# Performance work log

Measured on AMD Instinct MI355X. Metric: run time of the kernel, lower is better.

The kernel has to match this reference:

```python
import jax, jax.numpy as jnp
import numpy as np

B, H, W = 4, 256, 256
DIM, DIM_OUT, NUM_HEADS = 96, 192, 3
WS = 8            # window_size
QS = 2            # q_stride (2,2)
HIDDEN = int(DIM_OUT * 4.0)
EPS = 1e-6


def layernorm(x, g, b):
    m = jnp.mean(x, axis=-1, keepdims=True)
    v = jnp.mean(jnp.square(x - m), axis=-1, keepdims=True)
    return (x - m) * jax.lax.rsqrt(v + EPS) * g + b


def maxpool2x2(x):
    # x: [..., h, w, c] -> [..., h//2, w//2, c]
    s = x.shape
    x = x.reshape(s[:-3] + (s[-3] // QS, QS, s[-2] // QS, QS, s[-1]))
    return x.max(axis=(-4, -2))


def setup_inputs() -> dict:
    key = jax.random.key(0)
    ks = jax.random.split(key, 16)
    std = 0.02
    return {
        "x": jax.random.normal(ks[0], (B, H, W, DIM), dtype=jnp.float32),
        "norm1_g": jnp.ones((DIM,), jnp.float32),
        "norm1_b": jnp.zeros((DIM,), jnp.float32),
        "proj_w": jax.random.normal(ks[1], (DIM, DIM_OUT), jnp.float32) * std,
        "proj_b": jnp.zeros((DIM_OUT,), jnp.float32),
        "qkv_w": jax.random.normal(ks[2], (DIM, 3 * DIM_OUT), jnp.float32) * std,
        "qkv_b": jnp.zeros((3 * DIM_OUT,), jnp.float32),
        "attn_proj_w": jax.random.normal(ks[3], (DIM_OUT, DIM_OUT), jnp.float32) * std,
        "attn_proj_b": jnp.zeros((DIM_OUT,), jnp.float32),
        "norm2_g": jnp.ones((DIM_OUT,), jnp.float32),
        "norm2_b": jnp.zeros((DIM_OUT,), jnp.float32),
        "mlp_w1": jax.random.normal(ks[4], (DIM_OUT, HIDDEN), jnp.float32) * std,
        "mlp_b1": jnp.zeros((HIDDEN,), jnp.float32),
        "mlp_w2": jax.random.normal(ks[5], (HIDDEN, DIM_OUT), jnp.float32) * std,
        "mlp_b2": jnpp_zeros if False else jnp.zeros((DIM_OUT,), jnp.float32),
    }


def reference(x, norm1_g, norm1_b, proj_w, proj_b, qkv_w, qkv_b,
              attn_proj_w, attn_proj_b, norm2_g, norm2_b,
              mlp_w1, mlp_b1, mlp_w2, mlp_b2):
    b, h, w, _ = x.shape
    xn = layernorm(x, norm1_g, norm1_b)

    # dim != dim_out: shortcut = proj(norm(x)), then pooled by q_stride
    shortcut = xn @ proj_w + proj_b                       # [B,H,W,Do]
    shortcut = maxpool2x2(shortcut)                       # [B,H/2,W/2,Do]

    # window partition (H,W divisible by WS -> no padding)
    nh, nw = h // WS, w // WS
    xw = xn.reshape(b, nh, WS, nw, WS, DIM).transpose(0, 1, 3, 2, 4, 5)
    xw = xw.reshape(b * nh * nw, WS, WS, DIM)             # [Bw,WS,WS,C]
    Bw = xw.shape[0]

    # MultiScaleAttention with q pooling
    hd = DIM_OUT // NUM_HEADS
    qkv = (xw @ qkv_w + qkv_b).reshape(Bw, WS * WS, 3, NUM_HEADS, hd)
    q, k, v = qkv[:, :, 0], qkv[:, :, 1], qkv[:, :, 2]    # [Bw,N,h,d]
    q = maxpool2x2(q.reshape(Bw, WS, WS, DIM_OUT))        # [Bw,WS/2,WS/2,Do]
    wq = WS // QS
    q = q.reshape(Bw, wq * wq, NUM_HEADS, hd)

    scale = 1.0 / jnp.sqrt(jnp.asarray(hd, x.dtype))
    scores = jnp.einsum('bqhd,bkhd->bhqk', q, k) * scale
    probs = jax.nn.softmax(scores, axis=-1)
    out = jnp.einsum('bhqk,bkhd->bqhd', probs, v).reshape(Bw, wq, wq, DIM_OUT)
    out = out @ attn_proj_w + attn_proj_b                 # [Bw,wq,wq,Do]

    # window unpartition at pooled resolution
    hp, wp = h // QS, w // QS
    out = out.reshape(b, nh, nw, wq, wq, DIM_OUT).transpose(0, 1, 3, 2, 4, 5)
    out = out.reshape(b, hp, wp, DIM_OUT)

    y = shortcut + out
    yn = layernorm(y, norm2_g, norm2_b)
    mlp = jax.nn.gelu(yn @ mlp_w1 + mlp_b1, approximate=False) @ mlp_w2 + mlp_b2
    return y + mlp
```

## Files before the change

kernel.cpp:

```cpp
#include <hip/hip_runtime.h>
#include <hip/hip_bf16.h>
#include <math.h>

#define EPSV 1e-6f

typedef __attribute__((ext_vector_type(8))) short bf16x8;
typedef __attribute__((ext_vector_type(4))) float f32x4;
typedef __attribute__((ext_vector_type(4))) unsigned short u16x4;

__device__ inline float bf2f(unsigned short u) {
  union { unsigned int i; float f; } v;
  v.i = ((unsigned int)u) << 16;
  return v.f;
}
__device__ inline unsigned short f2bf(float f) {
  unsigned int u = __builtin_bit_cast(unsigned int, f);
  u += 0x7FFFu + ((u >> 16) & 1u);
  return (unsigned short)(u >> 16);
}
__device__ inline float fast_gelu(float v) {
  float u = 1.5957691216057308f * (v + 0.044715f * v * v * v);
  float t = __expf(-u);
  return v * __builtin_amdgcn_rcpf(1.f + t);
}

__global__ __launch_bounds__(256) void k0_pack(
    const float* __restrict__ qw, const float* __restrict__ aw,
    const float* __restrict__ w1, const float* __restrict__ w2,
    const float* __restrict__ pw, unsigned short* __restrict__ qwp,
    unsigned short* __restrict__ awp, unsigned short* __restrict__ w1p,
    unsigned short* __restrict__ w2p, unsigned short* __restrict__ pwp) {
  int idx = blockIdx.x * 256 + threadIdx.x;
  int lane = idx & 63;
  int l15 = lane & 15, quad = lane >> 4;
  if (idx < 6912) {
    int fi = idx >> 6;
    int ntile = fi / 3, kstep = fi - ntile * 3;
    int n = ntile * 16 + l15, k0 = kstep * 32 + quad * 8;
#pragma unroll
    for (int j = 0; j < 8; ++j)
      qwp[(size_t)idx * 8 + j] = f2bf(qw[(size_t)(k0 + j) * 576 + n]);
  } else if (idx < 11520) {
    int i2 = idx - 6912;
    int fi = i2 >> 6;
    int ntile = fi / 6, kstep = fi - ntile * 6;
    int n = ntile * 16 + l15, k0 = kstep * 32 + quad * 8;
#pragma unroll
    for (int j = 0; j < 8; ++j)
      awp[(size_t)i2 * 8 + j] = f2bf(aw[(size_t)(k0 + j) * 192 + n]);
  } else if (idx < 29952) {
    int i3 = idx - 11520;
    int fi = i3 >> 6;
    int ntile = fi / 6, kstep = fi - ntile * 6;
    int n = ntile * 16 + l15, k0 = kstep * 32 + quad * 8;
#pragma unroll
    for (int j = 0; j < 8; ++j)
      w1p[(size_t)i3 * 8 + j] = f2bf(w1[(size_t)(k0 + j) * 768 + n]);
  } else if (idx < 48384) {
    int i4 = idx - 29952;
    int fi = i4 >> 6;
    int ntile = fi / 24, kstep = fi - ntile * 24;
    int n = ntile * 16 + l15, k0 = kstep * 32 + quad * 8;
#pragma unroll
    for (int j = 0; j < 8; ++j)
      w2p[(size_t)i4 * 8 + j] = f2bf(w2[(size_t)(k0 + j) * 192 + n]);
  } else if (idx < 50688) {
    int i5 = idx - 48384;
    int fi = i5 >> 6;
    int ntile = fi / 3, kstep = fi - ntile * 3;
    int n = ntile * 16 + l15, k0 = kstep * 32 + quad * 8;
#pragma unroll
    for (int j = 0; j < 8; ++j)
      pwp[(size_t)i5 * 8 + j] = f2bf(pw[(size_t)(k0 + j) * 192 + n]);
  }
}

__global__ __launch_bounds__(256) void k1234_fused(
    const float* __restrict__ x, const float* __restrict__ n1g,
    const float* __restrict__ n1b, const unsigned short* __restrict__ pwp,
    const float* __restrict__ pb, const unsigned short* __restrict__ qwp,
    const float* __restrict__ qb, const unsigned short* __restrict__ awp,
    const float* __restrict__ ab, const float* __restrict__ n2g,
    const float* __restrict__ n2b, const unsigned short* __restrict__ w1p,
    const float* __restrict__ b1, const unsigned short* __restrict__ w2p,
    const float* __restrict__ b2, float* __restrict__ out) {
  __shared__ __align__(16) unsigned char smem[46848];
  unsigned short (*kk)[200] = (unsigned short (*)[200])smem;
  unsigned short (*vT)[72] = (unsigned short (*)[72])smem;
  unsigned short (*wbuf)[16][72] =
      (unsigned short (*)[16][72])(smem + 27648);
  float (*sc)[192] = (float (*)[192])(smem + 34560);
  unsigned short (*yn)[200] = (unsigned short (*)[200])(smem + 6400);
  unsigned short (*hls)[200] = (unsigned short (*)[200])(smem + 12800);

  int tid = threadIdx.x, wave = tid >> 6, lane = tid & 63;
  int wi = blockIdx.x;
  int b = wi >> 10, nh = (wi >> 5) & 31, nw = wi & 31;
  int grow0 = nh * 8, gcol0 = nw * 8;
  int l15 = lane & 15, quad = lane >> 4;

  {
    int tt = tid >> 2, sub = tid & 3;
    int rr = tt >> 3, cc = tt & 7;
    size_t tok = (size_t)((b * 256 + grow0 + rr) * 256 + gcol0 + cc);
    const f32x4* xr4 = (const f32x4*)(x + tok * 96 + sub * 24);
    f32x4 v[6];
#pragma unroll
    for (int i = 0; i < 6; ++i) v[i] = xr4[i];
    float s = 0.f;
#pragma unroll
    for (int i = 0; i < 6; ++i)
#pragma unroll
      for (int j = 0; j < 4; ++j) s += v[i][j];
    s += __shfl_xor(s, 1);
    s += __shfl_xor(s, 2);
    float mean = s * (1.f / 96.f);
    float q = 0.f;
#pragma unroll
    for (int i = 0; i < 6; ++i)
#pragma unroll
      for (int j = 0; j < 4; ++j) {
        float d = v[i][j] - mean;
        q += d * d;
      }
    q += __shfl_xor(q, 1);
    q += __shfl_xor(q, 2);
    float rstd = rsqrtf(q * (1.f / 96.f) + EPSV);
    const f32x4* g4 = (const f32x4*)(n1g + sub * 24);
    const f32x4* b4 = (const f32x4*)(n1b + sub * 24);
#pragma unroll
    for (int i = 0; i < 6; ++i) {
      f32x4 gg = g4[i], bb = b4[i];
      u16x4 o;
#pragma unroll
      for (int j = 0; j < 4; ++j)
        o[j] = f2bf((v[i][j] - mean) * rstd * gg[j] + bb[j]);
      *(u16x4*)(&kk[tt][sub * 24 + i * 4]) = o;
    }
  }
  __syncthreads();

  bf16x8 areg[4][3];
#pragma unroll
  for (int mt = 0; mt < 4; ++mt)
#pragma unroll
    for (int ks = 0; ks < 3; ++ks)
      areg[mt][ks] = *(const bf16x8*)(&kk[mt * 16 + l15][ks * 32 + quad * 8]);
  __syncthreads();

#pragma unroll
  for (int nl = 0; nl < 3; ++nl) {
    int nt = wave * 3 + nl;
    const unsigned short* bp = pwp + ((size_t)(nt * 3) * 64 + lane) * 8;
    bf16x8 b0 = *(const bf16x8*)(bp);
    bf16x8 b1v = *(const bf16x8*)(bp + 512);
    bf16x8 b2v = *(const bf16x8*)(bp + 1024);
    int c = nt * 16 + l15;
    float bias = pb[c];
#pragma unroll
    for (int mt = 0; mt < 4; ++mt) {
      f32x4 acc = {0.f, 0.f, 0.f, 0.f};
      acc = __builtin_amdgcn_mfma_f32_16x16x32_bf16(areg[mt][0], b0, acc, 0, 0, 0);
      acc = __builtin_amdgcn_mfma_f32_16x16x32_bf16(areg[mt][1], b1v, acc, 0, 0, 0);
      acc = __builtin_amdgcn_mfma_f32_16x16x32_bf16(areg[mt][2], b2v, acc, 0, 0, 0);
      float p0 = fmaxf(acc[0], acc[1]);
      float p1 = fmaxf(acc[2], acc[3]);
      float q0 = fmaxf(p0, __shfl_xor(p0, 32));
      float q1 = fmaxf(p1, __shfl_xor(p1, 32));
      if (quad < 2) {
        int p = mt * 4 + quad * 2;
        sc[p][c] = q0 + bias;
        sc[p + 1][c] = q1 + bias;
      }
    }
  }

#pragma unroll
  for (int aj = 0; aj < 6; ++aj) {
    int type, hh, nt;
    if (wave < 3) {
      if (aj < 4) { type = 0; hh = wave; nt = aj; }
      else { int kidx = wave * 2 + (aj - 4); type = 1; hh = kidx >> 2; nt = kidx & 3; }
    } else {
      int kidx = 6 + aj; type = 1; hh = kidx >> 2; nt = kidx & 3;
    }
    int gnt = type * 12 + hh * 4 + nt;
    const unsigned short* bp = qwp + (size_t)gnt * 1536 + lane * 8;
    bf16x8 b0 = *(const bf16x8*)(bp);
    bf16x8 b1v = *(const bf16x8*)(bp + 512);
    bf16x8 b2v = *(const bf16x8*)(bp + 1024);
    int dloc = nt * 16 + l15;
    int dglob = hh * 64 + dloc;
    float bias = qb[type * 192 + dglob];
#pragma unroll
    for (int mt = 0; mt < 4; ++mt) {
      f32x4 acc = {0.f, 0.f, 0.f, 0.f};
      acc = __builtin_amdgcn_mfma_f32_16x16x32_bf16(areg[mt][0], b0, acc, 0, 0, 0);
      acc = __builtin_amdgcn_mfma_f32_16x16x32_bf16(areg[mt][1], b1v, acc, 0, 0, 0);
      acc = __builtin_amdgcn_mfma_f32_16x16x32_bf16(areg[mt][2], b2v, acc, 0, 0, 0);
      if (type == 0) {
        float p0 = fmaxf(acc[0], acc[1]);
        float p1 = fmaxf(acc[2], acc[3]);
        float q0 = fmaxf(p0, __shfl_xor(p0, 32));
        float q1 = fmaxf(p1, __shfl_xor(p1, 32));
        if (quad < 2) {
          int p = mt * 4 + quad * 2;
          wbuf[wave][p][dloc] = f2bf(q0 + bias);
          wbuf[wave][p + 1][dloc] = f2bf(q1 + bias);
        }
      } else {
        int t0 = mt * 16 + quad * 4;
#pragma unroll
        for (int r = 0; r < 4; ++r) kk[t0 + r][dglob] = f2bf(acc[r] + bias);
      }
    }
  }
  __syncthreads();

  f32x4 s4[4];
  if (wave < 3) {
    int h = wave;
    bf16x8 aq0 = *(const bf16x8*)(&wbuf[wave][l15][quad * 8]);
    bf16x8 aq1 = *(const bf16x8*)(&wbuf[wave][l15][32 + quad * 8]);
#pragma unroll
    for (int kt = 0; kt < 4; ++kt) {
      bf16x8 bk0 = *(const bf16x8*)(&kk[kt * 16 + l15][h * 64 + quad * 8]);
      bf16x8 bk1 = *(const bf16x8*)(&kk[kt * 16 + l15][h * 64 + 32 + quad * 8]);
      f32x4 s = {0.f, 0.f, 0.f, 0.f};
      s = __builtin_amdgcn_mfma_f32_16x16x32_bf16(aq0, bk0, s, 0, 0, 0);
      s = __builtin_amdgcn_mfma_f32_16x16x32_bf16(aq1, bk1, s, 0, 0, 0);
      s4[kt] = s;
    }
  }
  __syncthreads();

#pragma unroll
  for (int vj = 0; vj < 3; ++vj) {
    int vidx = wave * 3 + vj;
    int hh = vidx >> 2, nt = vidx & 3;
    const unsigned short* bp =
        qwp + (size_t)(24 + hh * 4 + nt) * 1536 + lane * 8;
    bf16x8 b0 = *(const bf16x8*)(bp);
    bf16x8 b1v = *(const bf16x8*)(bp + 512);
    bf16x8 b2v = *(const bf16x8*)(bp + 1024);
    int dglob = hh * 64 + nt * 16 + l15;
    float bias = qb[384 + dglob];
#pragma unroll
    for (int mt = 0; mt < 4; ++mt) {
      f32x4 acc = {0.f, 0.f, 0.f, 0.f};
      acc = __builtin_amdgcn_mfma_f32_16x16x32_bf16(areg[mt][0], b0, acc, 0, 0, 0);
      acc = __builtin_amdgcn_mfma_f32_16x16x32_bf16(areg[mt][1], b1v, acc, 0, 0, 0);
      acc = __builtin_amdgcn_mfma_f32_16x16x32_bf16(areg[mt][2], b2v, acc, 0, 0, 0);
      int t0 = mt * 16 + quad * 4;
      u16x4 pk;
#pragma unroll
      for (int r = 0; r < 4; ++r) pk[r] = f2bf(acc[r] + bias);
      *(u16x4*)(&vT[dglob][t0]) = pk;
    }
  }

  if (wave < 3) {
    float ps[4][4];
#pragma unroll
    for (int r = 0; r < 4; ++r) {
      float m = fmaxf(fmaxf(s4[0][r], s4[1][r]), fmaxf(s4[2][r], s4[3][r]));
#pragma unroll
      for (int o = 8; o; o >>= 1) m = fmaxf(m, __shfl_xor(m, o));
      float sm = 0.f;
#pragma unroll
      for (int kt = 0; kt < 4; ++kt) {
        float e = __expf((s4[kt][r] - m) * 0.125f);
        ps[kt][r] = e;
        sm += e;
      }
#pragma unroll
      for (int o = 8; o; o >>= 1) sm += __shfl_xor(sm, o);
      float inv = __builtin_amdgcn_rcpf(sm);
#pragma unroll
      for (int kt = 0; kt < 4; ++kt) ps[kt][r] *= inv;
    }
#pragma unroll
    for (int kt = 0; kt < 4; ++kt)
#pragma unroll
      for (int r = 0; r < 4; ++r)
        wbuf[wave][quad * 4 + r][kt * 16 + l15] = f2bf(ps[kt][r]);
  }
  __syncthreads();

  f32x4 o4[4];
  if (wave < 3) {
    int h = wave;
    bf16x8 ap0 = *(const bf16x8*)(&wbuf[wave][l15][quad * 8]);
    bf16x8 ap1 = *(const bf16x8*)(&wbuf[wave][l15][32 + quad * 8]);
#pragma unroll
    for (int dt = 0; dt < 4; ++dt) {
      bf16x8 bv0 = *(const bf16x8*)(&vT[h * 64 + dt * 16 + l15][quad * 8]);
      bf16x8 bv1 = *(const bf16x8*)(&vT[h * 64 + dt * 16 + l15][32 + quad * 8]);
      f32x4 o = {0.f, 0.f, 0.f, 0.f};
      o = __builtin_amdgcn_mfma_f32_16x16x32_bf16(ap0, bv0, o, 0, 0, 0);
      o = __builtin_amdgcn_mfma_f32_16x16x32_bf16(ap1, bv1, o, 0, 0, 0);
      o4[dt] = o;
    }
  }
  __syncthreads();

  if (wave < 3) {
    int h = wave;
#pragma unroll
    for (int dt = 0; dt < 4; ++dt)
#pragma unroll
      for (int r = 0; r < 4; ++r)
        kk[quad * 4 + r][h * 64 + dt * 16 + l15] = f2bf(o4[dt][r]);
  }
  __syncthreads();

  bf16x8 ao[6];
#pragma unroll
  for (int ks = 0; ks < 6; ++ks)
    ao[ks] = *(const bf16x8*)(&kk[l15][ks * 32 + quad * 8]);
#pragma unroll
  for (int nl = 0; nl < 3; ++nl) {
    int ntl = wave * 3 + nl;
    const unsigned short* bp = awp + (size_t)ntl * 3072 + lane * 8;
    f32x4 acc = {0.f, 0.f, 0.f, 0.f};
#pragma unroll
    for (int ks = 0; ks < 6; ++ks) {
      bf16x8 bw = *(const bf16x8*)(bp + ks * 512);
      acc = __builtin_amdgcn_mfma_f32_16x16x32_bf16(ao[ks], bw, acc, 0, 0, 0);
    }
    int cc = ntl * 16 + l15;
    float bias = ab[cc];
#pragma unroll
    for (int r = 0; r < 4; ++r) {
      int p = quad * 4 + r;
      sc[p][cc] += acc[r] + bias;
    }
  }
  __syncthreads();

  {
    int tt = wave * 4 + quad;
    const f32x4* y4 = (const f32x4*)(&sc[tt][l15 * 12]);
    f32x4 vv[3];
    vv[0] = y4[0]; vv[1] = y4[1]; vv[2] = y4[2];
    float s = 0.f;
#pragma unroll
    for (int i = 0; i < 3; ++i)
#pragma unroll
      for (int j = 0; j < 4; ++j) s += vv[i][j];
    s += __shfl_xor(s, 1);
    s += __shfl_xor(s, 2);
    s += __shfl_xor(s, 4);
    s += __shfl_xor(s, 8);
    float mean = s * (1.f / 192.f);
    float q = 0.f;
#pragma unroll
    for (int i = 0; i < 3; ++i)
#pragma unroll
      for (int j = 0; j < 4; ++j) {
        float d = vv[i][j] - mean;
        q += d * d;
      }
    q += __shfl_xor(q, 1);
    q += __shfl_xor(q, 2);
    q += __shfl_xor(q, 4);
    q += __shfl_xor(q, 8);
    float rstd = rsqrtf(q * (1.f / 192.f) + EPSV);
    const f32x4* g4 = (const f32x4*)(n2g + l15 * 12);
    const f32x4* b4 = (const f32x4*)(n2b + l15 * 12);
#pragma unroll
    for (int i = 0; i < 3; ++i) {
      f32x4 gg = g4[i], bb = b4[i];
      u16x4 o;
#pragma unroll
      for (int j = 0; j < 4; ++j)
        o[j] = f2bf((vv[i][j] - mean) * rstd * gg[j] + bb[j]);
      *(u16x4*)(&yn[tt][l15 * 12 + i * 4]) = o;
    }
  }
  __syncthreads();

  bf16x8 ar[6];
#pragma unroll
  for (int ks = 0; ks < 6; ++ks)
    ar[ks] = *(const bf16x8*)(&yn[l15][ks * 32 + quad * 8]);

  f32x4 acc2[3];
#pragma unroll
  for (int nl = 0; nl < 3; ++nl) acc2[nl] = (f32x4){0.f, 0.f, 0.f, 0.f};

  for (int c = 0; c < 4; ++c) {
#pragma unroll
    for (int nl = 0; nl < 3; ++nl) {
      int gnt = c * 12 + wave * 3 + nl;
      const unsigned short* bp = w1p + ((size_t)(gnt * 6) * 64 + lane) * 8;
      f32x4 t0 = {0.f, 0.f, 0.f, 0.f};
#pragma unroll
      for (int ks = 0; ks < 6; ++ks) {
        bf16x8 bw = *(const bf16x8*)(bp + ks * 512);
        t0 = __builtin_amdgcn_mfma_f32_16x16x32_bf16(ar[ks], bw, t0, 0, 0, 0);
      }
      int lcol = wave * 48 + nl * 16 + l15;
      float bias = b1[c * 192 + lcol];
#pragma unroll
      for (int r = 0; r < 4; ++r)
        hls[quad * 4 + r][lcol] = f2bf(fast_gelu(t0[r] + bias));
    }
    __syncthreads();
    bf16x8 hr[6];
#pragma unroll
    for (int ks = 0; ks < 6; ++ks)
      hr[ks] = *(const bf16x8*)(&hls[l15][ks * 32 + quad * 8]);
#pragma unroll
    for (int nl = 0; nl < 3; ++nl) {
      int nt2 = wave * 3 + nl;
      const unsigned short* bp =
          w2p + ((size_t)(nt2 * 24 + c * 6) * 64 + lane) * 8;
#pragma unroll
      for (int ks = 0; ks < 6; ++ks) {
        bf16x8 bw = *(const bf16x8*)(bp + ks * 512);
        acc2[nl] =
            __builtin_amdgcn_mfma_f32_16x16x32_bf16(hr[ks], bw, acc2[nl], 0, 0, 0);
      }
    }
    __syncthreads();
  }

#pragma unroll
  for (int nl = 0; nl < 3; ++nl) {
    int col = (wave * 3 + nl) * 16 + l15;
    float bias = b2[col];
#pragma unroll
    for (int r = 0; r < 4; ++r) {
      int p = quad * 4 + r;
      int hp = nh * 4 + (p >> 2), wp2 = nw * 4 + (p & 3);
      size_t oi = ((size_t)((b * 128 + hp) * 128 + wp2)) * 192 + col;
      out[oi] = sc[p][col] + acc2[nl][r] + bias;
    }
  }
}

extern "C" void kernel_launch(void* const* d_in, const int* in_sizes, int n_in,
                              void* d_out, int out_size, void* d_ws,
                              size_t ws_size, hipStream_t stream) {
  const float* x = (const float*)d_in[0];
  const float* n1g = (const float*)d_in[1];
  const float* n1b = (const float*)d_in[2];
  const float* pw = (const float*)d_in[3];
  const float* pb = (const float*)d_in[4];
  const float* qw = (const float*)d_in[5];
  const float* qb = (const float*)d_in[6];
  const float* aw = (const float*)d_in[7];
  const float* ab = (const float*)d_in[8];
  const float* n2g = (const float*)d_in[9];
  const float* n2b = (const float*)d_in[10];
  const float* w1 = (const float*)d_in[11];
  const float* b1 = (const float*)d_in[12];
  const float* w2 = (const float*)d_in[13];
  const float* b2 = (const float*)d_in[14];
  float* out = (float*)d_out;

  char* wsb = (char*)d_ws;
  unsigned short* qwp = (unsigned short*)wsb;
  unsigned short* awp = (unsigned short*)(wsb + 110592);
  unsigned short* w1p = (unsigned short*)(wsb + 184320);
  unsigned short* w2p = (unsigned short*)(wsb + 479232);
  unsigned short* pwp = (unsigned short*)(wsb + 774144);

  hipLaunchKernelGGL(k0_pack, dim3(198), dim3(256), 0, stream, qw, aw, w1, w2,
                     pw, qwp, awp, w1p, w2p, pwp);
  hipLaunchKernelGGL(k1234_fused, dim3(4096), dim3(256), 0, stream, x, n1g,
                     n1b, pwp, pb, qwp, qb, awp, ab, n2g, n2b, w1p, b1, w2p,
                     b2, out);
}
```

Before: 317.8 us.

## Use hardware packed bf16 conversion and shrink LDS to fit more blocks

Replaces the software round-to-nearest f32-to-bf16 conversion with the v_cvt_pk_bf16_f32 instruction, which converts two values at once, at every staging point. The shortcut projection results are held in registers and written to LDS later, so the score buffer can alias the wbuf region and the shared allocation drops from 46848 to 39936 bytes. Launch bounds now request 4 blocks per CU to raise occupancy. The cost is extra live registers for the held shortcut values, under a tighter register budget that could cause spills.

```diff
diff --git a/kernel.cpp b/kernel.cpp
--- a/kernel.cpp
+++ b/kernel.cpp
@@ -7,6 +7,7 @@
 typedef __attribute__((ext_vector_type(8))) short bf16x8;
 typedef __attribute__((ext_vector_type(4))) float f32x4;
 typedef __attribute__((ext_vector_type(4))) unsigned short u16x4;
+typedef __attribute__((ext_vector_type(2))) unsigned int u32x2;
 
 __device__ inline float bf2f(unsigned short u) {
   union { unsigned int i; float f; } v;
@@ -17,6 +18,11 @@
   unsigned int u = __builtin_bit_cast(unsigned int, f);
   u += 0x7FFFu + ((u >> 16) & 1u);
   return (unsigned short)(u >> 16);
+}
+__device__ inline unsigned int pk2(float lo, float hi) {
+  unsigned int r;
+  asm("v_cvt_pk_bf16_f32 %0, %1, %2" : "=v"(r) : "v"(lo), "v"(hi));
+  return r;
 }
 __device__ inline float fast_gelu(float v) {
   float u = 1.5957691216057308f * (v + 0.044715f * v * v * v);
@@ -75,7 +81,7 @@
   }
 }
 
-__global__ __launch_bounds__(256) void k1234_fused(
+__global__ __launch_bounds__(256, 4) void k1234_fused(
     const float* __restrict__ x, const float* __restrict__ n1g,
     const float* __restrict__ n1b, const unsigned short* __restrict__ pwp,
     const float* __restrict__ pb, const unsigned short* __restrict__ qwp,
@@ -84,14 +90,14 @@
     const float* __restrict__ n2b, const unsigned short* __restrict__ w1p,
     const float* __restrict__ b1, const unsigned short* __restrict__ w2p,
     const float* __restrict__ b2, float* __restrict__ out) {
-  __shared__ __align__(16) unsigned char smem[46848];
+  __shared__ __align__(16) unsigned char smem[39936];
   unsigned short (*kk)[200] = (unsigned short (*)[200])smem;
   unsigned short (*vT)[72] = (unsigned short (*)[72])smem;
+  unsigned short (*yn)[200] = (unsigned short (*)[200])(smem + 6400);
+  unsigned short (*hls)[200] = (unsigned short (*)[200])(smem + 12800);
   unsigned short (*wbuf)[16][72] =
       (unsigned short (*)[16][72])(smem + 27648);
-  float (*sc)[192] = (float (*)[192])(smem + 34560);
-  unsigned short (*yn)[200] = (unsigned short (*)[200])(smem + 6400);
-  unsigned short (*hls)[200] = (unsigned short (*)[200])(smem + 12800);
+  float (*sc)[192] = (float (*)[192])(smem + 27648);
 
   int tid = threadIdx.x, wave = tid >> 6, lane = tid & 63;
   int wi = blockIdx.x;
@@ -131,11 +137,12 @@
 #pragma unroll
     for (int i = 0; i < 6; ++i) {
       f32x4 gg = g4[i], bb = b4[i];
-      u16x4 o;
-#pragma unroll
-      for (int j = 0; j < 4; ++j)
-        o[j] = f2bf((v[i][j] - mean) * rstd * gg[j] + bb[j]);
-      *(u16x4*)(&kk[tt][sub * 24 + i * 4]) = o;
+      u32x2 w;
+      w[0] = pk2((v[i][0] - mean) * rstd * gg[0] + bb[0],
+                 (v[i][1] - mean) * rstd * gg[1] + bb[1]);
+      w[1] = pk2((v[i][2] - mean) * rstd * gg[2] + bb[2],
+                 (v[i][3] - mean) * rstd * gg[3] + bb[3]);
+      *(u32x2*)(&kk[tt][sub * 24 + i * 4]) = w;
     }
   }
   __syncthreads();
@@ -148,6 +155,7 @@
       areg[mt][ks] = *(const bf16x8*)(&kk[mt * 16 + l15][ks * 32 + quad * 8]);
   __syncthreads();
 
+  float scr[3][4][2];
 #pragma unroll
   for (int nl = 0; nl < 3; ++nl) {
     int nt = wave * 3 + nl;
@@ -155,8 +163,7 @@
     bf16x8 b0 = *(const bf16x8*)(bp);
     bf16x8 b1v = *(const bf16x8*)(bp + 512);
     bf16x8 b2v = *(const bf16x8*)(bp + 1024);
-    int c = nt * 16 + l15;
-    float bias = pb[c];
+    float bias = pb[nt * 16 + l15];
 #pragma unroll
     for (int mt = 0; mt < 4; ++mt) {
       f32x4 acc = {0.f, 0.f, 0.f, 0.f};
@@ -165,13 +172,8 @@
       acc = __builtin_amdgcn_mfma_f32_16x16x32_bf16(areg[mt][2], b2v, acc, 0, 0, 0);
       float p0 = fmaxf(acc[0], acc[1]);
       float p1 = fmaxf(acc[2], acc[3]);
-      float q0 = fmaxf(p0, __shfl_xor(p0, 32));
-      float q1 = fmaxf(p1, __shfl_xor(p1, 32));
-      if (quad < 2) {
-        int p = mt * 4 + quad * 2;
-        sc[p][c] = q0 + bias;
-        sc[p + 1][c] = q1 + bias;
-      }
+      scr[nl][mt][0] = fmaxf(p0, __shfl_xor(p0, 32)) + bias;
+      scr[nl][mt][1] = fmaxf(p1, __shfl_xor(p1, 32)) + bias;
     }
   }
 
@@ -203,15 +205,20 @@
         float p1 = fmaxf(acc[2], acc[3]);
         float q0 = fmaxf(p0, __shfl_xor(p0, 32));
         float q1 = fmaxf(p1, __shfl_xor(p1, 32));
+        unsigned int uq = pk2(q0 + bias, q1 + bias);
         if (quad < 2) {
           int p = mt * 4 + quad * 2;
-          wbuf[wave][p][dloc] = f2bf(q0 + bias);
-          wbuf[wave][p + 1][dloc] = f2bf(q1 + bias);
+          wbuf[wave][p][dloc] = (unsigned short)uq;
+          wbuf[wave][p + 1][dloc] = (unsigned short)(uq >> 16);
         }
       } else {
         int t0 = mt * 16 + quad * 4;
-#pragma unroll
-        for (int r = 0; r < 4; ++r) kk[t0 + r][dglob] = f2bf(acc[r] + bias);
+        unsigned int u01 = pk2(acc[0] + bias, acc[1] + bias);
+        unsigned int u23 = pk2(acc[2] + bias, acc[3] + bias);
+        kk[t0 + 0][dglob] = (unsigned short)u01;
+        kk[t0 + 1][dglob] = (unsigned short)(u01 >> 16);
+        kk[t0 + 2][dglob] = (unsigned short)u23;
+        kk[t0 + 3][dglob] = (unsigned short)(u23 >> 16);
       }
     }
   }
@@ -252,10 +259,10 @@
       acc = __builtin_amdgcn_mfma_f32_16x16x32_bf16(areg[mt][1], b1v, acc, 0, 0, 0);
       acc = __builtin_amdgcn_mfma_f32_16x16x32_bf16(areg[mt][2], b2v, acc, 0, 0, 0);
       int t0 = mt * 16 + quad * 4;
-      u16x4 pk;
-#pragma unroll
-      for (int r = 0; r < 4; ++r) pk[r] = f2bf(acc[r] + bias);
-      *(u16x4*)(&vT[dglob][t0]) = pk;
+      u32x2 pk;
+      pk[0] = pk2(acc[0] + bias, acc[1] + bias);
+      pk[1] = pk2(acc[2] + bias, acc[3] + bias);
+      *(u32x2*)(&vT[dglob][t0]) = pk;
     }
   }
 
@@ -280,10 +287,15 @@
       for (int kt = 0; kt < 4; ++kt) ps[kt][r] *= inv;
     }
 #pragma unroll
-    for (int kt = 0; kt < 4; ++kt)
-#pragma unroll
-      for (int r = 0; r < 4; ++r)
-        wbuf[wave][quad * 4 + r][kt * 16 + l15] = f2bf(ps[kt][r]);
+    for (int r = 0; r < 4; ++r) {
+      int row = quad * 4 + r;
+      unsigned int u0 = pk2(ps[0][r], ps[1][r]);
+      unsigned int u1 = pk2(ps[2][r], ps[3][r]);
+      wbuf[wave][row][l15] = (unsigned short)u0;
+      wbuf[wave][row][16 + l15] = (unsigned short)(u0 >> 16);
+      wbuf[wave][row][32 + l15] = (unsigned short)u1;
+      wbuf[wave][row][48 + l15] = (unsigned short)(u1 >> 16);
+    }
   }
   __syncthreads();
 
@@ -307,10 +319,27 @@
   if (wave < 3) {
     int h = wave;
 #pragma unroll
-    for (int dt = 0; dt < 4; ++dt)
-#pragma unroll
-      for (int r = 0; r < 4; ++r)
-        kk[quad * 4 + r][h * 64 + dt * 16 + l15] = f2bf(o4[dt][r]);
+    for (int r = 0; r < 4; ++r) {
+      int row = quad * 4 + r;
+      unsigned int u0 = pk2(o4[0][r], o4[1][r]);
+      unsigned int u1 = pk2(o4[2][r], o4[3][r]);
+      kk[row][h * 64 + l15] = (unsigned short)u0;
+      kk[row][h * 64 + 16 + l15] = (unsigned short)(u0 >> 16);
+      kk[row][h * 64 + 32 + l15] = (unsigned short)u1;
+      kk[row][h * 64 + 48 + l15] = (unsigned short)(u1 >> 16);
+    }
+  }
+  if (quad < 2) {
+#pragma unroll
+    for (int nl = 0; nl < 3; ++nl) {
+      int c = (wave * 3 + nl) * 16 + l15;
+#pragma unroll
+      for (int mt = 0; mt < 4; ++mt) {
+        int p = mt * 4 + quad * 2;
+        sc[p][c] = scr[nl][mt][0];
+        sc[p + 1][c] = scr[nl][mt][1];
+      }
+    }
   }
   __syncthreads();
 
@@ -371,11 +400,12 @@
 #pragma unroll
     for (int i = 0; i < 3; ++i) {
       f32x4 gg = g4[i], bb = b4[i];
-      u16x4 o;
-#pragma unroll
-      for (int j = 0; j < 4; ++j)
-        o[j] = f2bf((vv[i][j] - mean) * rstd * gg[j] + bb[j]);
-      *(u16x4*)(&yn[tt][l15 * 12 + i * 4]) = o;
+      u32x2 w;
+      w[0] = pk2((vv[i][0] - mean) * rstd * gg[0] + bb[0],
+                 (vv[i][1] - mean) * rstd * gg[1] + bb[1]);
+      w[1] = pk2((vv[i][2] - mean) * rstd * gg[2] + bb[2],
+                 (vv[i][3] - mean) * rstd * gg[3] + bb[3]);
+      *(u32x2*)(&yn[tt][l15 * 12 + i * 4]) = w;
     }
   }
   __syncthreads();
@@ -402,9 +432,12 @@
       }
       int lcol = wave * 48 + nl * 16 + l15;
       float bias = b1[c * 192 + lcol];
-#pragma unroll
-      for (int r = 0; r < 4; ++r)
-        hls[quad * 4 + r][lcol] = f2bf(fast_gelu(t0[r] + bias));
+      unsigned int u0 = pk2(fast_gelu(t0[0] + bias), fast_gelu(t0[1] + bias));
+      unsigned int u1 = pk2(fast_gelu(t0[2] + bias), fast_gelu(t0[3] + bias));
+      hls[quad * 4 + 0][lcol] = (unsigned short)u0;
+      hls[quad * 4 + 1][lcol] = (unsigned short)(u0 >> 16);
+      hls[quad * 4 + 2][lcol] = (unsigned short)u1;
+      hls[quad * 4 + 3][lcol] = (unsigned short)(u1 >> 16);
     }
     __syncthreads();
     bf16x8 hr[6];
```

Result: slower. 368.7 us (+16.0%).
